# Optimization experiments

Measured on AMD Instinct MI355X. Metric: run time of the kernel, lower is better.

Reference implementation:

```python
import jax, jax.numpy as jnp
import numpy as np

B, N, F = 64, 512, 30          # batch, pf candidates, raw features
NDIM0, NDIM = 2, 4             # coord dims: layer0 uses 2, rest use n_dim_gnn=4
NOUT, NLAYERS = 64, 5          # GNN layer width / count
NDENSE = 128
BN_EPS = 1e-3                  # keras BatchNormalization default epsilon


def setup_inputs() -> dict:
    key = jax.random.key(0)
    ks = jax.random.split(key, 20)
    xx = jax.random.normal(ks[0], (B, N, F), jnp.float32)
    # validity mask: first L_b candidates valid
    lengths = jax.random.randint(ks[1], (B,), N // 4, N + 1)
    valid = (jnp.arange(N)[None, :] < lengths[:, None]).astype(jnp.float32)
    pt = jax.random.randint(ks[2], (B, N), 0, 8).astype(jnp.float32)
    pvq = jax.random.randint(ks[3], (B, N), 0, 8).astype(jnp.float32)
    fpv = jax.random.randint(ks[4], (B, N), 0, 4).astype(jnp.float32)
    xx = xx.at[:, :, 0].set(valid).at[:, :, 27].set(pt).at[:, :, 28].set(pvq).at[:, :, 29].set(fpv)
    g = lambda k, s, sc=0.05: jax.random.normal(k, s, jnp.float32) * sc
    d_in0 = 33  # 2+2+2 embeddings + 27 float features
    return {
        "xx": xx,
        "emb1": g(ks[5], (8, 2), 0.5),
        "emb2": g(ks[6], (8, 2), 0.5),
        "emb3": g(ks[7], (4, 2), 0.5),
        "A0": g(ks[8], ((d_in0 + 1) * 2 - 1, NOUT)),   # [67,64]
        "b0": g(ks[9], (NOUT,)),
        "A_rest": g(ks[10], (NLAYERS - 1, (NOUT + 1) * 2 - 1, NOUT)),  # [4,129,64]
        "b_rest": g(ks[11], (NLAYERS - 1, NOUT)),
        "bn_gamma": jnp.ones((NLAYERS, NOUT), jnp.float32),
        "bn_beta": jnp.zeros((NLAYERS, NOUT), jnp.float32),
        "dW0": g(ks[12], (N * NOUT, NDENSE), 0.01),
        "db0": g(ks[13], (NDENSE,)),
        "dW1": g(ks[14], (NDENSE, NDENSE)),
        "db1": g(ks[15], (NDENSE,)),
        "dbn_gamma": jnp.ones((2, NDENSE), jnp.float32),
        "dbn_beta": jnp.zeros((2, NDENSE), jnp.float32),
        "W2": g(ks[16], (NDENSE, 2)),
        "b2": g(ks[17], (2,)),
    }


def _bn(x, g, b):
    # inference BatchNorm with moving_mean=0, moving_var=1 (initial stats)
    return g * x * (1.0 / jnp.sqrt(1.0 + BN_EPS)) + b


def _gnn_layer(x, mask, n_dim, A, b):
    # x: [B,N,Fin], mask: [B,N]. Original builds [B,N,N,Fin+1] via tile/reshape;
    # algebraically the reduction over senders i factorizes:
    #   ss_feat[b,j] = x[b,j] * mask[b,j] * sum_i exp(-10*d_ij)
    #   ss_last[b,j] = mask[b,j] * sum_i d_ij * exp(-10*d_ij)
    c = x[..., -n_dim:]
    diff = c[:, :, None, :] - c[:, None, :, :]      # [B,N,N,n_dim]
    dist = jnp.sum(diff * diff, axis=-1)            # [B,N,N] squared distance
    w = jnp.exp(-10.0 * dist)
    S = jnp.sum(w, axis=1)                          # [B,N] per receiver j
    T = jnp.sum(dist * w, axis=1)                   # [B,N]
    ss_feat = x * (mask * S)[..., None] - x         # subtract concat(x, 0)
    ss_last = (mask * T)[..., None]
    xcat = jnp.concatenate([x, ss_feat, ss_last], axis=-1)  # [B,N,2*Fin+1]
    return (xcat @ A + b) * mask[..., None]


def _forward(xx, emb1, emb2, emb3, A0, b0, A_rest, b_rest, bn_gamma, bn_beta,
             dW0, db0, dW1, db1, dbn_gamma, dbn_beta, W2, b2):
    mask = xx[:, :, 0]
    e1 = emb1[jnp.abs(xx[:, :, 27]).astype(jnp.int32)]
    e2 = emb2[jnp.abs(xx[:, :, 28]).astype(jnp.int32)]
    e3 = emb3[jnp.abs(xx[:, :, 29]).astype(jnp.int32)]
    x = jnp.concatenate([e1, e2, e3, xx[:, :, :27]], axis=-1)  # [B,N,33]
    x = jnp.tanh(_bn(_gnn_layer(x, mask, NDIM0, A0, b0), bn_gamma[0], bn_beta[0]))
    for k in range(NLAYERS - 1):
        x = _gnn_layer(x, mask, NDIM, A_rest[k], b_rest[k])
        x = jnp.tanh(_bn(x, bn_gamma[k + 1], bn_beta[k + 1]))
    x = x.reshape(B, N * NOUT)
    x = jax.nn.sigmoid(_bn(x @ dW0 + db0, dbn_gamma[0], dbn_beta[0]))
    x = jax.nn.sigmoid(_bn(x @ dW1 + db1, dbn_gamma[1], dbn_beta[1]))
    x = x @ W2 + b2                                  # [B,2]
    # mode == 'dm': concat zeros on the right
    return jnp.concatenate([x, jnp.zeros((B, 2), x.dtype)], axis=1)


def reference(xx, emb1, emb2, emb3, A0, b0, A_rest, b_rest, bn_gamma, bn_beta,
              dW0, db0, dW1, db1, dbn_gamma, dbn_beta, W2, b2):
    return _forward(xx, emb1, emb2, emb3, A0, b0, A_rest, b_rest, bn_gamma, bn_beta,
                    dW0, db0, dW1, db1, dbn_gamma, dbn_beta, W2, b2)
```

## Files before the change

### kernel.cpp

```cpp
#include <hip/hip_runtime.h>
#include <math.h>

#define B_ 64
#define N_ 512
#define R_ (B_*N_)
#define INV_S 0.9995003746877732f

__device__ __forceinline__ float fast_tanh(float y){
  return 1.f - 2.f*__builtin_amdgcn_rcpf(1.f + __expf(2.f*y));
}
__device__ __forceinline__ float fast_sigmoid(float v){
  return __builtin_amdgcn_rcpf(1.f + __expf(-v));
}

struct GnnArgs {
  const float* xx;
  const float* emb1; const float* emb2; const float* emb3;
  const float* A0;  const float* b0;
  const float* Ar;  const float* br;
  const float* bng; const float* bnb;
  float4* cb0; float4* cb1;
  unsigned int* bar;
  float* xfinal;
};

__global__ void bar_init(unsigned int* bar)
{
  bar[threadIdx.x * 32] = 0u;
}

__global__ __launch_bounds__(512, 4) void gnn_fused(GnnArgs g)
{
  __shared__ float alo[64*64];
  __shared__ float ahi[64*64];
  __shared__ float xs[64*68];
  __shared__ float4 cl[512];
  __shared__ float spart[512], tpart[512];
  __shared__ float scl[64], tcl[64], ml[64];

  const int tid   = threadIdx.x;
  const int b     = blockIdx.x;
  const int jc    = blockIdx.y;
  const int jloc  = jc*64;
  const int rbase = b*N_;
  const int cg = tid & 15, rg = tid >> 4;
  const int o0 = cg*4,  lr0 = rg*2;
  unsigned int* barp = g.bar + b*32;

  for (int k = 0; k < 5; ++k){
    const float* A;  const float* bi;  int K, KP;
    if (k == 0){ A = g.A0;                        bi = g.b0;            K = 33; KP = 36; }
    else       { A = g.Ar + (size_t)(k-1)*129*64; bi = g.br + (k-1)*64; K = 64; KP = 64; }
    const float* gam = g.bng + k*64;
    const float* bet = g.bnb + k*64;

    if (k == 0){
      for (int idx = tid; idx < 36*64; idx += 512){
        int f = idx >> 6;
        alo[idx] = (f < 33) ? A[idx] : 0.f;
        ahi[idx] = (f < 33) ? A[33*64 + idx] : 0.f;
      }
      {
        const float* xr = g.xx + (size_t)(rbase + tid)*30;
        cl[tid] = make_float4(xr[25], xr[26], 0.f, 0.f);
      }
      if (tid < 64){
        const float* row = g.xx + (size_t)(rbase + jloc + tid)*30;
        float v[30];
#pragma unroll
        for (int i=0;i<30;i++) v[i] = row[i];
        int i1 = (int)fabsf(v[27]);
        int i2 = (int)fabsf(v[28]);
        int i3 = (int)fabsf(v[29]);
        float* o = &xs[tid*68];
        o[0]=g.emb1[i1*2+0]; o[1]=g.emb1[i1*2+1];
        o[2]=g.emb2[i2*2+0]; o[3]=g.emb2[i2*2+1];
        o[4]=g.emb3[i3*2+0]; o[5]=g.emb3[i3*2+1];
#pragma unroll
        for (int i=0;i<27;i++) o[6+i] = v[i];
        o[33]=0.f; o[34]=0.f; o[35]=0.f;
        ml[tid] = v[0];
      }
    } else {
      __syncthreads();
      if (tid == 0){
        __builtin_amdgcn_fence(__ATOMIC_RELEASE, "agent");
        __hip_atomic_fetch_add(barp, 1u, __ATOMIC_RELAXED, __HIP_MEMORY_SCOPE_AGENT);
      }
      {
        const float4* A4 = (const float4*)A;
        float4* alo4 = (float4*)alo;
        float4* ahi4 = (float4*)ahi;
        for (int idx = tid; idx < 1024; idx += 512){
          alo4[idx] = A4[idx];
          ahi4[idx] = A4[1024 + idx];
        }
      }
      if (tid == 0){
        unsigned int tgt = 8u*(unsigned int)k;
        while (__hip_atomic_load(barp, __ATOMIC_RELAXED, __HIP_MEMORY_SCOPE_AGENT) < tgt)
          __builtin_amdgcn_s_sleep(2);
        __builtin_amdgcn_fence(__ATOMIC_ACQUIRE, "agent");
      }
      __syncthreads();
      const float4* cbr = ((k & 1) ? g.cb0 : g.cb1) + rbase;
      cl[tid] = cbr[tid];
    }
    __syncthreads();

    {
      int jj = tid & 63, ic = tid >> 6, base = ic*64;
      float4 cj = cl[jloc + jj];
      float Ss = 0.f, Ts = 0.f;
#pragma unroll 8
      for (int i=0;i<64;i++){
        float4 ci = cl[base+i];
        float d0 = cj.x-ci.x, d1 = cj.y-ci.y, d2 = cj.z-ci.z, d3 = cj.w-ci.w;
        float dist = d0*d0 + d1*d1 + d2*d2 + d3*d3;
        float w = __expf(-10.f*dist);
        Ss += w; Ts += dist*w;
      }
      spart[tid] = Ss;
      tpart[tid] = Ts;
    }
    __syncthreads();

    if (tid < 64){
      float S = 0.f, T = 0.f;
#pragma unroll
      for (int c=0;c<8;c++){
        S += spart[tid + 64*c];
        T += tpart[tid + 64*c];
      }
      float m = ml[tid];
      scl[tid] = m*S - 1.f;
      tcl[tid] = m*T;
    }
    __syncthreads();

    float4 acc1[2], acc2[2];
#pragma unroll
    for (int rr=0;rr<2;rr++){
      acc1[rr] = make_float4(0.f,0.f,0.f,0.f);
      acc2[rr] = make_float4(0.f,0.f,0.f,0.f);
    }
#pragma unroll 2
    for (int kc = 0; kc < KP; kc += 4){
      float4 a1[4], a2[4], xv[2];
#pragma unroll
      for (int uu=0;uu<4;uu++){
        a1[uu] = *(const float4*)&alo[(kc+uu)*64 + o0];
        a2[uu] = *(const float4*)&ahi[(kc+uu)*64 + o0];
      }
#pragma unroll
      for (int rr=0;rr<2;rr++)
        xv[rr] = *(const float4*)&xs[(lr0+rr)*68 + kc];
#pragma unroll
      for (int uu=0;uu<4;uu++){
#pragma unroll
        for (int rr=0;rr<2;rr++){
          float xu = ((const float*)&xv[rr])[uu];
          acc1[rr].x = fmaf(xu, a1[uu].x, acc1[rr].x);
          acc1[rr].y = fmaf(xu, a1[uu].y, acc1[rr].y);
          acc1[rr].z = fmaf(xu, a1[uu].z, acc1[rr].z);
          acc1[rr].w = fmaf(xu, a1[uu].w, acc1[rr].w);
          acc2[rr].x = fmaf(xu, a2[uu].x, acc2[rr].x);
          acc2[rr].y = fmaf(xu, a2[uu].y, acc2[rr].y);
          acc2[rr].z = fmaf(xu, a2[uu].z, acc2[rr].z);
          acc2[rr].w = fmaf(xu, a2[uu].w, acc2[rr].w);
        }
      }
    }
    __syncthreads();

    float4 alast = *(const float4*)&A[(size_t)2*K*64 + o0];
    float4 bo = *(const float4*)&bi[o0];
    float4 go = *(const float4*)&gam[o0];
    float4 bb = *(const float4*)&bet[o0];
    float4* cbw = (k & 1) ? g.cb1 : g.cb0;
#pragma unroll
    for (int rr=0;rr<2;rr++){
      int lr = lr0 + rr;
      int r = rbase + jloc + lr;
      float sc = scl[lr], tc = tcl[lr], m = ml[lr];
      float4 v;
      v.x = (acc1[rr].x + sc*acc2[rr].x + tc*alast.x + bo.x)*m;
      v.y = (acc1[rr].y + sc*acc2[rr].y + tc*alast.y + bo.y)*m;
      v.z = (acc1[rr].z + sc*acc2[rr].z + tc*alast.z + bo.z)*m;
      v.w = (acc1[rr].w + sc*acc2[rr].w + tc*alast.w + bo.w)*m;
      float4 t;
      t.x = fast_tanh(go.x*(v.x*INV_S) + bb.x);
      t.y = fast_tanh(go.y*(v.y*INV_S) + bb.y);
      t.z = fast_tanh(go.z*(v.z*INV_S) + bb.z);
      t.w = fast_tanh(go.w*(v.w*INV_S) + bb.w);
      if (k < 4){
        *(float4*)&xs[lr*68 + o0] = t;
        if (cg == 15) cbw[r] = t;
      } else {
        *(float4*)&g.xfinal[(size_t)r*64 + o0] = t;
      }
    }
  }
}

__global__ __launch_bounds__(256) void dense0_partial(
    const float* __restrict__ X, const float* __restrict__ W,
    float* __restrict__ partial)
{
  __shared__ float xt[64*32];
  __shared__ float wt[32*128];
  int tid = threadIdx.x;
  int k0 = blockIdx.x*128;
  int og = (tid & 15)*8;
  int rg = (tid >> 4)*4;
  float acc[4][8];
#pragma unroll
  for (int a=0;a<4;a++)
#pragma unroll
    for (int u=0;u<8;u++) acc[a][u]=0.f;
  for (int kt = 0; kt < 128; kt += 32){
    __syncthreads();
    for (int idx = tid; idx < 512; idx += 256){
      int r = idx >> 3, kq = idx & 7;
      *(float4*)&xt[r*32 + kq*4] =
          *(const float4*)&X[(size_t)r*32768 + k0 + kt + kq*4];
    }
    {
      const float4* Wc = (const float4*)&W[(size_t)(k0+kt)*128];
      float4* wt4 = (float4*)wt;
      for (int idx = tid; idx < 1024; idx += 256) wt4[idx] = Wc[idx];
    }
    __syncthreads();
#pragma unroll 4
    for (int k=0;k<32;k++){
      float4 w0 = *(const float4*)&wt[k*128 + og];
      float4 w1 = *(const float4*)&wt[k*128 + og + 4];
      float xv[4];
#pragma unroll
      for (int rr=0;rr<4;rr++) xv[rr] = xt[(rg+rr)*32 + k];
#pragma unroll
      for (int rr=0;rr<4;rr++){
        acc[rr][0] = fmaf(xv[rr], w0.x, acc[rr][0]);
        acc[rr][1] = fmaf(xv[rr], w0.y, acc[rr][1]);
        acc[rr][2] = fmaf(xv[rr], w0.z, acc[rr][2]);
        acc[rr][3] = fmaf(xv[rr], w0.w, acc[rr][3]);
        acc[rr][4] = fmaf(xv[rr], w1.x, acc[rr][4]);
        acc[rr][5] = fmaf(xv[rr], w1.y, acc[rr][5]);
        acc[rr][6] = fmaf(xv[rr], w1.z, acc[rr][6]);
        acc[rr][7] = fmaf(xv[rr], w1.w, acc[rr][7]);
      }
    }
  }
  float* pb = partial + (size_t)blockIdx.x*8192;
#pragma unroll
  for (int rr=0;rr<4;rr++){
    *(float4*)&pb[(rg+rr)*128 + og]     = *(float4*)&acc[rr][0];
    *(float4*)&pb[(rg+rr)*128 + og + 4] = *(float4*)&acc[rr][4];
  }
}

__global__ __launch_bounds__(256) void dense_head(
    const float* __restrict__ partial,
    const float* __restrict__ db0, const float* __restrict__ dg0,
    const float* __restrict__ dbb0,
    const float* __restrict__ dW1, const float* __restrict__ db1,
    const float* __restrict__ dg1, const float* __restrict__ dbb1,
    const float* __restrict__ W2, const float* __restrict__ b2,
    float* __restrict__ out)
{
  __shared__ float sred[256];
  __shared__ float h[128];
  __shared__ float red0[128], red1[128];
  int tid = threadIdx.x;
  int b = blockIdx.x;
  int o = tid & 127, ph = tid >> 7;
  float s = 0.f;
#pragma unroll 16
  for (int p = ph*128; p < ph*128+128; p++)
    s += partial[(size_t)p*8192 + b*128 + o];
  sred[tid] = s;
  __syncthreads();
  if (tid < 128){
    float sum = sred[tid] + sred[tid+128];
    float v = dg0[tid]*((sum + db0[tid])*INV_S) + dbb0[tid];
    h[tid] = fast_sigmoid(v);
  }
  __syncthreads();
  if (tid < 128){
    float acc = 0.f;
#pragma unroll 8
    for (int k=0;k<128;k++) acc = fmaf(h[k], dW1[k*128 + tid], acc);
    float v = dg1[tid]*((acc + db1[tid])*INV_S) + dbb1[tid];
    float h1 = fast_sigmoid(v);
    red0[tid] = h1 * W2[tid*2+0];
    red1[tid] = h1 * W2[tid*2+1];
  }
  __syncthreads();
  for (int st=64; st>0; st>>=1){
    if (tid < st){ red0[tid] += red0[tid+st]; red1[tid] += red1[tid+st]; }
    __syncthreads();
  }
  if (tid == 0){
    out[b*4+0] = red0[0] + b2[0];
    out[b*4+1] = red1[0] + b2[1];
    out[b*4+2] = 0.f;
    out[b*4+3] = 0.f;
  }
}

extern "C" void kernel_launch(void* const* d_in, const int* in_sizes, int n_in,
                              void* d_out, int out_size, void* d_ws, size_t ws_size,
                              hipStream_t stream)
{
  const float* xx   = (const float*)d_in[0];
  const float* emb1 = (const float*)d_in[1];
  const float* emb2 = (const float*)d_in[2];
  const float* emb3 = (const float*)d_in[3];
  const float* A0   = (const float*)d_in[4];
  const float* b0   = (const float*)d_in[5];
  const float* Ar   = (const float*)d_in[6];
  const float* br   = (const float*)d_in[7];
  const float* bng  = (const float*)d_in[8];
  const float* bnb  = (const float*)d_in[9];
  const float* dW0  = (const float*)d_in[10];
  const float* db0  = (const float*)d_in[11];
  const float* dW1  = (const float*)d_in[12];
  const float* db1  = (const float*)d_in[13];
  const float* dbg  = (const float*)d_in[14];
  const float* dbb  = (const float*)d_in[15];
  const float* W2   = (const float*)d_in[16];
  const float* b2   = (const float*)d_in[17];

  float* ws = (float*)d_ws;
  float*  xA      = ws;
  float*  partial = xA + (size_t)R_*64;
  float4* cb0     = (float4*)(partial + (size_t)256*8192);
  float4* cb1     = cb0 + R_;
  unsigned int* bar = (unsigned int*)(cb1 + R_);

  bar_init<<<1, 64, 0, stream>>>(bar);

  GnnArgs ga;
  ga.xx = xx; ga.emb1 = emb1; ga.emb2 = emb2; ga.emb3 = emb3;
  ga.A0 = A0; ga.b0 = b0; ga.Ar = Ar; ga.br = br;
  ga.bng = bng; ga.bnb = bnb;
  ga.cb0 = cb0; ga.cb1 = cb1; ga.bar = bar; ga.xfinal = xA;

  hipLaunchKernelGGL(gnn_fused, dim3(64,8), dim3(512), 0, stream, ga);

  dense0_partial<<<256, 256, 0, stream>>>(xA, dW0, partial);
  dense_head<<<B_, 256, 0, stream>>>(partial, db0, dbg, dbb,
                                     dW1, db1, dbg + 128, dbb + 128,
                                     W2, b2, (float*)d_out);
}
```

Measured before the change: 220.9 us.

## Split GNN rows across more blocks, read weights from global, overlap matmul with barrier

The fused GNN kernel now gives each block 32 rows instead of 64, doubling the grid to 64x16 blocks and raising launch bounds to 8 blocks per CU. The A weight tiles are no longer staged in shared memory but read directly from global/cache per thread. The x·A matmul is moved before the inter-block barrier wait, so the GEMM overlaps with waiting for other blocks' coordinates. Layer 0 also gets a 2-dim distance loop. The cost is more redundant weight loads from global, and twice as many blocks taking part in each per-batch barrier.

```diff
diff --git a/kernel.cpp b/kernel.cpp
--- a/kernel.cpp
+++ b/kernel.cpp
@@ -29,22 +29,20 @@
   bar[threadIdx.x * 32] = 0u;
 }
 
-__global__ __launch_bounds__(512, 4) void gnn_fused(GnnArgs g)
-{
-  __shared__ float alo[64*64];
-  __shared__ float ahi[64*64];
-  __shared__ float xs[64*68];
+__global__ __launch_bounds__(512, 8) void gnn_fused(GnnArgs g)
+{
+  __shared__ float xs[32*68];
   __shared__ float4 cl[512];
-  __shared__ float spart[512], tpart[512];
-  __shared__ float scl[64], tcl[64], ml[64];
+  __shared__ float spart[256], tpart[256];
+  __shared__ float scl[32], tcl[32], ml[32];
 
   const int tid   = threadIdx.x;
   const int b     = blockIdx.x;
   const int jc    = blockIdx.y;
-  const int jloc  = jc*64;
+  const int jloc  = jc*32;
   const int rbase = b*N_;
   const int cg = tid & 15, rg = tid >> 4;
-  const int o0 = cg*4,  lr0 = rg*2;
+  const int o0 = cg*4;
   unsigned int* barp = g.bar + b*32;
 
   for (int k = 0; k < 5; ++k){
@@ -55,16 +53,11 @@
     const float* bet = g.bnb + k*64;
 
     if (k == 0){
-      for (int idx = tid; idx < 36*64; idx += 512){
-        int f = idx >> 6;
-        alo[idx] = (f < 33) ? A[idx] : 0.f;
-        ahi[idx] = (f < 33) ? A[33*64 + idx] : 0.f;
-      }
       {
         const float* xr = g.xx + (size_t)(rbase + tid)*30;
         cl[tid] = make_float4(xr[25], xr[26], 0.f, 0.f);
       }
-      if (tid < 64){
+      if (tid < 32){
         const float* row = g.xx + (size_t)(rbase + jloc + tid)*30;
         float v[30];
 #pragma unroll
@@ -81,120 +74,121 @@
         o[33]=0.f; o[34]=0.f; o[35]=0.f;
         ml[tid] = v[0];
       }
+      __syncthreads();
     } else {
       __syncthreads();
       if (tid == 0){
         __builtin_amdgcn_fence(__ATOMIC_RELEASE, "agent");
         __hip_atomic_fetch_add(barp, 1u, __ATOMIC_RELAXED, __HIP_MEMORY_SCOPE_AGENT);
       }
-      {
-        const float4* A4 = (const float4*)A;
-        float4* alo4 = (float4*)alo;
-        float4* ahi4 = (float4*)ahi;
-        for (int idx = tid; idx < 1024; idx += 512){
-          alo4[idx] = A4[idx];
-          ahi4[idx] = A4[1024 + idx];
+    }
+
+    float4 acc1 = make_float4(0.f,0.f,0.f,0.f);
+    float4 acc2 = make_float4(0.f,0.f,0.f,0.f);
+    {
+      const float4* A4 = (const float4*)A;
+      const float* xrow = &xs[rg*68];
+#pragma unroll 1
+      for (int kc = 0; kc < KP; kc += 4){
+        float4 a1[4], a2[4];
+#pragma unroll
+        for (int uu=0;uu<4;uu++){
+          bool ok = (kc+uu) < K;
+          a1[uu] = ok ? A4[(kc+uu)*16 + cg]
+                      : make_float4(0.f,0.f,0.f,0.f);
+          a2[uu] = ok ? A4[(K + kc+uu)*16 + cg]
+                      : make_float4(0.f,0.f,0.f,0.f);
         }
-      }
-      if (tid == 0){
-        unsigned int tgt = 8u*(unsigned int)k;
-        while (__hip_atomic_load(barp, __ATOMIC_RELAXED, __HIP_MEMORY_SCOPE_AGENT) < tgt)
-          __builtin_amdgcn_s_sleep(2);
-        __builtin_amdgcn_fence(__ATOMIC_ACQUIRE, "agent");
-      }
-      __syncthreads();
-      const float4* cbr = ((k & 1) ? g.cb0 : g.cb1) + rbase;
-      cl[tid] = cbr[tid];
-    }
-    __syncthreads();
-
-    {
-      int jj = tid & 63, ic = tid >> 6, base = ic*64;
-      float4 cj = cl[jloc + jj];
-      float Ss = 0.f, Ts = 0.f;
-#pragma unroll 8
-      for (int i=0;i<64;i++){
-        float4 ci = cl[base+i];
-        float d0 = cj.x-ci.x, d1 = cj.y-ci.y, d2 = cj.z-ci.z, d3 = cj.w-ci.w;
-        float dist = d0*d0 + d1*d1 + d2*d2 + d3*d3;
-        float w = __expf(-10.f*dist);
-        Ss += w; Ts += dist*w;
-      }
-      spart[tid] = Ss;
-      tpart[tid] = Ts;
-    }
-    __syncthreads();
-
-    if (tid < 64){
-      float S = 0.f, T = 0.f;
-#pragma unroll
-      for (int c=0;c<8;c++){
-        S += spart[tid + 64*c];
-        T += tpart[tid + 64*c];
-      }
-      float m = ml[tid];
-      scl[tid] = m*S - 1.f;
-      tcl[tid] = m*T;
-    }
-    __syncthreads();
-
-    float4 acc1[2], acc2[2];
-#pragma unroll
-    for (int rr=0;rr<2;rr++){
-      acc1[rr] = make_float4(0.f,0.f,0.f,0.f);
-      acc2[rr] = make_float4(0.f,0.f,0.f,0.f);
-    }
-#pragma unroll 2
-    for (int kc = 0; kc < KP; kc += 4){
-      float4 a1[4], a2[4], xv[2];
-#pragma unroll
-      for (int uu=0;uu<4;uu++){
-        a1[uu] = *(const float4*)&alo[(kc+uu)*64 + o0];
-        a2[uu] = *(const float4*)&ahi[(kc+uu)*64 + o0];
-      }
-#pragma unroll
-      for (int rr=0;rr<2;rr++)
-        xv[rr] = *(const float4*)&xs[(lr0+rr)*68 + kc];
-#pragma unroll
-      for (int uu=0;uu<4;uu++){
-#pragma unroll
-        for (int rr=0;rr<2;rr++){
-          float xu = ((const float*)&xv[rr])[uu];
-          acc1[rr].x = fmaf(xu, a1[uu].x, acc1[rr].x);
-          acc1[rr].y = fmaf(xu, a1[uu].y, acc1[rr].y);
-          acc1[rr].z = fmaf(xu, a1[uu].z, acc1[rr].z);
-          acc1[rr].w = fmaf(xu, a1[uu].w, acc1[rr].w);
-          acc2[rr].x = fmaf(xu, a2[uu].x, acc2[rr].x);
-          acc2[rr].y = fmaf(xu, a2[uu].y, acc2[rr].y);
-          acc2[rr].z = fmaf(xu, a2[uu].z, acc2[rr].z);
-          acc2[rr].w = fmaf(xu, a2[uu].w, acc2[rr].w);
+        float4 xv = *(const float4*)&xrow[kc];
+#pragma unroll
+        for (int uu=0;uu<4;uu++){
+          float xu = ((const float*)&xv)[uu];
+          acc1.x = fmaf(xu, a1[uu].x, acc1.x);
+          acc1.y = fmaf(xu, a1[uu].y, acc1.y);
+          acc1.z = fmaf(xu, a1[uu].z, acc1.z);
+          acc1.w = fmaf(xu, a1[uu].w, acc1.w);
+          acc2.x = fmaf(xu, a2[uu].x, acc2.x);
+          acc2.y = fmaf(xu, a2[uu].y, acc2.y);
+          acc2.z = fmaf(xu, a2[uu].z, acc2.z);
+          acc2.w = fmaf(xu, a2[uu].w, acc2.w);
         }
       }
     }
-    __syncthreads();
-
     float4 alast = *(const float4*)&A[(size_t)2*K*64 + o0];
     float4 bo = *(const float4*)&bi[o0];
     float4 go = *(const float4*)&gam[o0];
     float4 bb = *(const float4*)&bet[o0];
-    float4* cbw = (k & 1) ? g.cb1 : g.cb0;
-#pragma unroll
-    for (int rr=0;rr<2;rr++){
-      int lr = lr0 + rr;
-      int r = rbase + jloc + lr;
-      float sc = scl[lr], tc = tcl[lr], m = ml[lr];
+
+    if (k >= 1){
+      if (tid == 0){
+        unsigned int tgt = 16u*(unsigned int)k;
+        while (__hip_atomic_load(barp, __ATOMIC_RELAXED, __HIP_MEMORY_SCOPE_AGENT) < tgt)
+          __builtin_amdgcn_s_sleep(2);
+        __builtin_amdgcn_fence(__ATOMIC_ACQUIRE, "agent");
+      }
+      __syncthreads();
+      const float4* cbr = ((k & 1) ? g.cb0 : g.cb1) + rbase;
+      cl[tid] = cbr[tid];
+      __syncthreads();
+    }
+
+    if (tid < 256){
+      int jj = tid & 31, ic = tid >> 5, base = ic*64;
+      float4 cj = cl[jloc + jj];
+      float Ss = 0.f, Ts = 0.f;
+      if (k == 0){
+#pragma unroll 8
+        for (int i=0;i<64;i++){
+          float4 ci = cl[base+i];
+          float d0 = cj.x-ci.x, d1 = cj.y-ci.y;
+          float dist = d0*d0 + d1*d1;
+          float w = __expf(-10.f*dist);
+          Ss += w; Ts += dist*w;
+        }
+      } else {
+#pragma unroll 8
+        for (int i=0;i<64;i++){
+          float4 ci = cl[base+i];
+          float d0 = cj.x-ci.x, d1 = cj.y-ci.y, d2 = cj.z-ci.z, d3 = cj.w-ci.w;
+          float dist = d0*d0 + d1*d1 + d2*d2 + d3*d3;
+          float w = __expf(-10.f*dist);
+          Ss += w; Ts += dist*w;
+        }
+      }
+      spart[jj + 32*ic] = Ss;
+      tpart[jj + 32*ic] = Ts;
+    }
+    __syncthreads();
+
+    if (tid < 32){
+      float S = 0.f, T = 0.f;
+#pragma unroll
+      for (int c=0;c<8;c++){
+        S += spart[tid + 32*c];
+        T += tpart[tid + 32*c];
+      }
+      float m = ml[tid];
+      scl[tid] = m*S - 1.f;
+      tcl[tid] = m*T;
+    }
+    __syncthreads();
+
+    {
+      float sc = scl[rg], tc = tcl[rg], m = ml[rg];
       float4 v;
-      v.x = (acc1[rr].x + sc*acc2[rr].x + tc*alast.x + bo.x)*m;
-      v.y = (acc1[rr].y + sc*acc2[rr].y + tc*alast.y + bo.y)*m;
-      v.z = (acc1[rr].z + sc*acc2[rr].z + tc*alast.z + bo.z)*m;
-      v.w = (acc1[rr].w + sc*acc2[rr].w + tc*alast.w + bo.w)*m;
+      v.x = (acc1.x + sc*acc2.x + tc*alast.x + bo.x)*m;
+      v.y = (acc1.y + sc*acc2.y + tc*alast.y + bo.y)*m;
+      v.z = (acc1.z + sc*acc2.z + tc*alast.z + bo.z)*m;
+      v.w = (acc1.w + sc*acc2.w + tc*alast.w + bo.w)*m;
       float4 t;
       t.x = fast_tanh(go.x*(v.x*INV_S) + bb.x);
       t.y = fast_tanh(go.y*(v.y*INV_S) + bb.y);
       t.z = fast_tanh(go.z*(v.z*INV_S) + bb.z);
       t.w = fast_tanh(go.w*(v.w*INV_S) + bb.w);
+      int r = rbase + jloc + rg;
       if (k < 4){
-        *(float4*)&xs[lr*68 + o0] = t;
+        *(float4*)&xs[rg*68 + o0] = t;
+        float4* cbw = (k & 1) ? g.cb1 : g.cb0;
         if (cg == 15) cbw[r] = t;
       } else {
         *(float4*)&g.xfinal[(size_t)r*64 + o0] = t;
@@ -346,7 +340,7 @@
   ga.bng = bng; ga.bnb = bnb;
   ga.cb0 = cb0; ga.cb1 = cb1; ga.bar = bar; ga.xfinal = xA;
 
-  hipLaunchKernelGGL(gnn_fused, dim3(64,8), dim3(512), 0, stream, ga);
+  hipLaunchKernelGGL(gnn_fused, dim3(64,16), dim3(512), 0, stream, ga);
 
   dense0_partial<<<256, 256, 0, stream>>>(xA, dW0, partial);
   dense_head<<<B_, 256, 0, stream>>>(partial, db0, dbg, dbb,
```

After: 350.9 us. 1.59x slower.
